# Kernel optimization log

Measured on AMD Instinct MI355X. Metric: run time of the kernel, lower is better.

The kernel has to match this reference:

```python
import jax, jax.numpy as jnp
import numpy as np

N_STATES = 2048   # number of hidden states
N_OBS = 8192      # emission alphabet size
T = 8192          # sequence length


def setup_inputs() -> dict:
    key = jax.random.key(0)
    k1, k2, k3, k4 = jax.random.split(key, 4)
    Pi_0 = jax.random.uniform(k1, (N_STATES,), jnp.float32)
    Pi_0 = Pi_0 / Pi_0.sum()  # initial distribution
    A = jax.random.uniform(k2, (N_STATES, N_STATES), jnp.float32)
    A = A / A.sum(axis=1, keepdims=True)  # row-stochastic transition matrix
    # emission values scaled so the per-step multiplicative factor has mean ~1,
    # keeping alpha numerically stable over T steps (the raw algorithm never rescales)
    B = jax.random.uniform(k3, (N_STATES, N_OBS), jnp.float32) * 2.0
    se = jax.random.randint(k4, (T,), 0, N_OBS)
    return {"Pi_0": Pi_0, "A": A, "B": B, "se": se}


def reference(Pi_0, A, B, se):
    # HMM forward algorithm:
    #   alpha_0[i] = Pi_0[i] * B[i, se[0]]
    #   alpha_t[i] = (sum_j alpha_{t-1}[j] * A[j, i]) * B[i, se[t]]
    #   return -log(sum_i alpha_T[i])
    Bobs = B[:, se].T            # [T, n_states] emission prob of each observed symbol
    alpha0 = Pi_0 * Bobs[0]      # [n_states]

    def step(alpha, b_t):
        alpha = (alpha @ A) * b_t  # vectorized recurrence: matvec + elementwise
        return alpha, None

    alpha, _ = jax.lax.scan(step, alpha0, Bobs[1:])
    return -jnp.log(jnp.sum(alpha))
```

## Files before the change

### kernel.cpp

```cpp
#include <hip/hip_runtime.h>
#include <hip/hip_bf16.h>
#include <math.h>


#define NS    2048
#define NOBS  8192
#define TSEQ  8192
#define NBLK  64
#define NTHR  512
#define OPB   32
#define JPT   128

typedef unsigned long long u64;
typedef unsigned int u32;

#define A_LIST(X) \
  X(0)  X(1)  X(2)  X(3)  X(4)  X(5)  X(6)  X(7)  \
  X(8)  X(9)  X(10) X(11) X(12) X(13) X(14) X(15) \
  X(16) X(17) X(18) X(19) X(20) X(21) X(22) X(23) \
  X(24) X(25) X(26) X(27) X(28) X(29) X(30) X(31)

__global__ void __launch_bounds__(256) init_ws_kernel(u64* aG) {
  const int i = blockIdx.x * 256 + threadIdx.x;
#pragma unroll
  for (int c = 0; c < 4; ++c) {
    __hip_atomic_store(&aG[i * 4 + c], 0ull, __ATOMIC_RELAXED, __HIP_MEMORY_SCOPE_AGENT);
  }
}

__global__ void __launch_bounds__(NTHR, 2) hmm_forward_kernel(
    const float* __restrict__ Pi0,
    const float* __restrict__ A,
    const float* __restrict__ B,
    const int*   __restrict__ se,
    float* __restrict__ out,
    u64*   __restrict__ aG) {
  __shared__ __align__(16) float alpha_sm[NS];
  __shared__ float red[2][NTHR / 64][OPB];

  const int tid    = threadIdx.x;
  const int blk    = blockIdx.x;
  const int w      = tid >> 6;
  const int lane   = tid & 63;
  const int h      = lane >> 5;
  const int o      = lane & 31;
  const int i_mine = blk * OPB + o;
  const int jbase  = (w * 2 + h) * JPT;

#define DECLA(k) float4 Ar##k;
  A_LIST(DECLA)
#define LOADA(k) { const float* ap = A + (size_t)(jbase + 4 * k) * NS + i_mine; \
                   Ar##k.x = ap[0]; Ar##k.y = ap[NS]; Ar##k.z = ap[2 * NS]; Ar##k.w = ap[3 * NS]; }
  A_LIST(LOADA)
#define PIN4(k) asm volatile("" : "+v"(Ar##k.x), "+v"(Ar##k.y), "+v"(Ar##k.z), "+v"(Ar##k.w));
  A_LIST(PIN4)

  {
    const int s0 = se[0];
#pragma unroll
    for (int c = 0; c < 4; ++c) {
      const int i = tid * 4 + c;
      alpha_sm[i] = Pi0[i] * B[(size_t)i * NOBS + s0];
    }
  }
  __syncthreads();

  float bv_next = 0.f;
  if (tid < OPB) bv_next = B[(size_t)i_mine * NOBS + se[1]];

  for (int t = 1; t < TSEQ; ++t) {
    const float bv  = bv_next;
    const int   buf = t & 1;
    if (tid < OPB) {
      const int tn = (t + 1 < TSEQ) ? (t + 1) : t;
      bv_next = B[(size_t)i_mine * NOBS + se[tn]];
    }

    float a0 = 0.f, a1 = 0.f, a2 = 0.f, a3 = 0.f;
#define DOT(k) { const float4 av = *reinterpret_cast<const float4*>(&alpha_sm[jbase + 4 * k]); \
                 a0 = fmaf(Ar##k.x, av.x, a0); a1 = fmaf(Ar##k.y, av.y, a1); \
                 a2 = fmaf(Ar##k.z, av.z, a2); a3 = fmaf(Ar##k.w, av.w, a3); }
    A_LIST(DOT)
    float acc = (a0 + a1) + (a2 + a3);
    acc += __shfl_xor(acc, 32);
    if (lane < 32) red[buf][w][o] = acc;
    __syncthreads();

    if (w == 0) {
      float s = 0.f;
#pragma unroll
      for (int ww = 0; ww < NTHR / 64; ++ww) s += red[buf][ww][o];
      if (lane < 32) {
        const float aval = s * bv;
        const u64 pkt = (u64)__float_as_uint(aval) | ((u64)(u32)t << 32);
        __hip_atomic_store(&aG[(size_t)buf * NS + blk * OPB + o], pkt,
                           __ATOMIC_RELAXED, __HIP_MEMORY_SCOPE_AGENT);
      }
    }

    {
      const u64* src = aG + (size_t)buf * NS + w * 256 + lane * 4;
      u64 q0, q1, q2, q3;
      const u32 tag = (u32)t;
      for (;;) {
        q0 = __hip_atomic_load(&src[0], __ATOMIC_RELAXED, __HIP_MEMORY_SCOPE_AGENT);
        q1 = __hip_atomic_load(&src[1], __ATOMIC_RELAXED, __HIP_MEMORY_SCOPE_AGENT);
        q2 = __hip_atomic_load(&src[2], __ATOMIC_RELAXED, __HIP_MEMORY_SCOPE_AGENT);
        q3 = __hip_atomic_load(&src[3], __ATOMIC_RELAXED, __HIP_MEMORY_SCOPE_AGENT);
        if ((u32)(q0 >> 32) == tag && (u32)(q1 >> 32) == tag &&
            (u32)(q2 >> 32) == tag && (u32)(q3 >> 32) == tag) break;
      }
      float4 v;
      v.x = __uint_as_float((u32)q0);
      v.y = __uint_as_float((u32)q1);
      v.z = __uint_as_float((u32)q2);
      v.w = __uint_as_float((u32)q3);
      *reinterpret_cast<float4*>(&alpha_sm[w * 256 + lane * 4]) = v;
    }
  }

  if (blk == 0) {
    __syncthreads();
    float s = 0.f;
#pragma unroll
    for (int c = 0; c < 4; ++c) s += alpha_sm[4 * tid + c];
#pragma unroll
    for (int off = 32; off > 0; off >>= 1) s += __shfl_xor(s, off);
    if (lane == 0) red[0][w][0] = s;
    __syncthreads();
    if (tid == 0) {
      float S = 0.f;
#pragma unroll
      for (int ww = 0; ww < NTHR / 64; ++ww) S += red[0][ww][0];
      out[0] = -logf(S);
    }
  }
}

extern "C" void kernel_launch(void* const* d_in, const int* in_sizes, int n_in,
                              void* d_out, int out_size, void* d_ws, size_t ws_size,
                              hipStream_t stream) {
  const float* Pi0 = (const float*)d_in[0];
  const float* A   = (const float*)d_in[1];
  const float* B   = (const float*)d_in[2];
  const int*   se  = (const int*)d_in[3];
  float*       out = (float*)d_out;

  u64* aG = (u64*)d_ws;

  init_ws_kernel<<<4, 256, 0, stream>>>(aG);
  hmm_forward_kernel<<<NBLK, NTHR, 0, stream>>>(Pi0, A, B, se, out, aG);
}
```

Baseline: 17.47 ms.

## Replace tagged 64-bit alpha packets with separate data array and per-block flags

Each block now publishes its alpha slice as plain 32-bit values, waits for those stores to complete, and then writes a single per-block step flag padded to its own cache line. Consumers poll only the 8 flags covering their wavefront's range and then read the data with 64-bit loads. Previously every element carried a 32-bit step tag and consumers polled all of them, so this halves the data traffic and shrinks the polling set. In exchange, publishing adds a serializing wait before the flag store, and correctness now depends on relaxed-ordering visibility of the data before the flag.

```diff
diff --git a/kernel.cpp b/kernel.cpp
--- a/kernel.cpp
+++ b/kernel.cpp
@@ -10,6 +10,7 @@
 #define NTHR  512
 #define OPB   32
 #define JPT   128
+#define FSTR  32
 
 typedef unsigned long long u64;
 typedef unsigned int u32;
@@ -20,11 +21,11 @@
   X(16) X(17) X(18) X(19) X(20) X(21) X(22) X(23) \
   X(24) X(25) X(26) X(27) X(28) X(29) X(30) X(31)
 
-__global__ void __launch_bounds__(256) init_ws_kernel(u64* aG) {
-  const int i = blockIdx.x * 256 + threadIdx.x;
+__global__ void __launch_bounds__(256) init_ws_kernel(u32* flags) {
+  const int i = threadIdx.x;
 #pragma unroll
-  for (int c = 0; c < 4; ++c) {
-    __hip_atomic_store(&aG[i * 4 + c], 0ull, __ATOMIC_RELAXED, __HIP_MEMORY_SCOPE_AGENT);
+  for (int c = 0; c < 8; ++c) {
+    __hip_atomic_store(&flags[i * 8 + c], 0u, __ATOMIC_RELAXED, __HIP_MEMORY_SCOPE_AGENT);
   }
 }
 
@@ -34,7 +35,8 @@
     const float* __restrict__ B,
     const int*   __restrict__ se,
     float* __restrict__ out,
-    u64*   __restrict__ aG) {
+    u32*   __restrict__ aGd,
+    u32*   __restrict__ flags) {
   __shared__ __align__(16) float alpha_sm[NS];
   __shared__ float red[2][NTHR / 64][OPB];
 
@@ -91,30 +93,40 @@
 #pragma unroll
       for (int ww = 0; ww < NTHR / 64; ++ww) s += red[buf][ww][o];
       if (lane < 32) {
-        const float aval = s * bv;
-        const u64 pkt = (u64)__float_as_uint(aval) | ((u64)(u32)t << 32);
-        __hip_atomic_store(&aG[(size_t)buf * NS + blk * OPB + o], pkt,
+        __hip_atomic_store(&aGd[(size_t)buf * NS + blk * OPB + o],
+                           __float_as_uint(s * bv),
+                           __ATOMIC_RELAXED, __HIP_MEMORY_SCOPE_AGENT);
+      }
+      asm volatile("s_waitcnt vmcnt(0)" ::: "memory");
+      if (lane == 0) {
+        __hip_atomic_store(&flags[blk * FSTR], (u32)t,
                            __ATOMIC_RELAXED, __HIP_MEMORY_SCOPE_AGENT);
       }
     }
 
     {
-      const u64* src = aG + (size_t)buf * NS + w * 256 + lane * 4;
-      u64 q0, q1, q2, q3;
-      const u32 tag = (u32)t;
+      const int srcb = 8 * w + (lane & 7);
       for (;;) {
-        q0 = __hip_atomic_load(&src[0], __ATOMIC_RELAXED, __HIP_MEMORY_SCOPE_AGENT);
-        q1 = __hip_atomic_load(&src[1], __ATOMIC_RELAXED, __HIP_MEMORY_SCOPE_AGENT);
-        q2 = __hip_atomic_load(&src[2], __ATOMIC_RELAXED, __HIP_MEMORY_SCOPE_AGENT);
-        q3 = __hip_atomic_load(&src[3], __ATOMIC_RELAXED, __HIP_MEMORY_SCOPE_AGENT);
-        if ((u32)(q0 >> 32) == tag && (u32)(q1 >> 32) == tag &&
-            (u32)(q2 >> 32) == tag && (u32)(q3 >> 32) == tag) break;
+        u32 fv = 0u;
+        if (lane < 8) {
+          fv = __hip_atomic_load(&flags[srcb * FSTR],
+                                 __ATOMIC_RELAXED, __HIP_MEMORY_SCOPE_AGENT);
+        }
+        const bool ok = (lane < 8) ? (fv >= (u32)t) : true;
+        if (__ballot(ok) == ~0ull) break;
       }
+    }
+
+    {
+      const u64* dsrc = reinterpret_cast<const u64*>(
+          aGd + (size_t)buf * NS + w * 256 + lane * 4);
+      const u64 d0 = __hip_atomic_load(dsrc + 0, __ATOMIC_RELAXED, __HIP_MEMORY_SCOPE_AGENT);
+      const u64 d1 = __hip_atomic_load(dsrc + 1, __ATOMIC_RELAXED, __HIP_MEMORY_SCOPE_AGENT);
       float4 v;
-      v.x = __uint_as_float((u32)q0);
-      v.y = __uint_as_float((u32)q1);
-      v.z = __uint_as_float((u32)q2);
-      v.w = __uint_as_float((u32)q3);
+      v.x = __uint_as_float((u32)d0);
+      v.y = __uint_as_float((u32)(d0 >> 32));
+      v.z = __uint_as_float((u32)d1);
+      v.w = __uint_as_float((u32)(d1 >> 32));
       *reinterpret_cast<float4*>(&alpha_sm[w * 256 + lane * 4]) = v;
     }
   }
@@ -146,8 +158,9 @@
   const int*   se  = (const int*)d_in[3];
   float*       out = (float*)d_out;
 
-  u64* aG = (u64*)d_ws;
+  u32* aGd   = (u32*)d_ws;
+  u32* flags = (u32*)((char*)d_ws + 16384);
 
-  init_ws_kernel<<<4, 256, 0, stream>>>(aG);
-  hmm_forward_kernel<<<NBLK, NTHR, 0, stream>>>(Pi0, A, B, se, out, aG);
+  init_ws_kernel<<<1, 256, 0, stream>>>(flags);
+  hmm_forward_kernel<<<NBLK, NTHR, 0, stream>>>(Pi0, A, B, se, out, aGd, flags);
 }
```

New measurement: 18.33 ms. 5.0% more time.
